# Kernel optimization log

Measured on AMD Instinct MI355X. Metric: run time of the kernel, lower is better.

## Reference

```python
import jax, jax.numpy as jnp
import numpy as np

B, T, N = 8, 168, 1024
FD, FS, FF = 16, 32, 8
DL, DG, HE, E = 128, 128, 4, 16384
BN = B * N


def _lstm_last(x, Wih, Whh, bih, bhh):
    # x: (BN, T, FD); PyTorch gate order i, f, g, o
    h0 = jnp.zeros((x.shape[0], Whh.shape[1]), x.dtype)
    def step(carry, xt):
        h, c = carry
        g = xt @ Wih.T + h @ Whh.T + bih + bhh
        i, f, gg, o = jnp.split(g, 4, axis=-1)
        c = jax.nn.sigmoid(f) * c + jax.nn.sigmoid(i) * jnp.tanh(gg)
        h = jax.nn.sigmoid(o) * jnp.tanh(c)
        return (h, c), None
    (h, _), _ = jax.lax.scan(step, (h0, h0), jnp.swapaxes(x, 0, 1))
    return h


def _ln(x, g, b):
    mu = x.mean(-1, keepdims=True)
    v = ((x - mu) ** 2).mean(-1, keepdims=True)
    return (x - mu) / jnp.sqrt(v + 1e-5) * g + b


def _gat(x, src, dst, ea, W, a_src, a_dst, a_edge, We, bias):
    # PyG GATConv: concat=False (mean over heads), edge_dim=1, LeakyReLU(0.2)
    xl = (x @ W.T).reshape(BN, HE, -1)                 # (BN, H, C)
    as_ = jnp.sum(xl * a_src, -1)                      # (BN, H)
    ad_ = jnp.sum(xl * a_dst, -1)
    ep = (ea @ We.T).reshape(-1, HE, xl.shape[-1])     # (Eb, H, C)
    ae_ = jnp.sum(ep * a_edge, -1)                     # (Eb, H)
    alpha = jax.nn.leaky_relu(as_[src] + ad_[dst] + ae_, 0.2)
    amax = jax.ops.segment_max(alpha, dst, num_segments=BN)
    ex = jnp.exp(alpha - amax[dst])
    den = jax.ops.segment_sum(ex, dst, num_segments=BN)
    w = ex / den[dst]                                  # softmax over incoming edges
    out = jax.ops.segment_sum(w[:, :, None] * xl[src], dst, num_segments=BN)
    return out.mean(axis=1) + bias


def _forward(fl, edge_index):
    (dyn, fcst, sta, ew,
     lWih, lWhh, lbih, lbhh, sW, sb, fW, fb, uW, ub,
     g0W, g0as, g0ad, g0ae, g0We, g0b,
     g1W, g1as, g1ad, g1ae, g1We, g1b,
     n0g, n0b, n1g, n1b, oW, ob) = fl
    x = jnp.transpose(dyn, (0, 2, 1, 3)).reshape(BN, T, FD)
    z = _lstm_last(x, lWih, lWhh, lbih, lbhh)
    s = jax.nn.relu(sta.reshape(BN, -1) @ sW.T + sb)
    f = jax.nn.relu(fcst.reshape(BN, -1) @ fW.T + fb)
    h = jax.nn.relu(jnp.concatenate([z, s, f], -1) @ uW.T + ub)
    # batch the graph: B disjoint copies with node offsets
    off = (jnp.arange(B) * N)[:, None]
    src = (edge_index[0][None] + off).reshape(-1)
    dst = (edge_index[1][None] + off).reshape(-1)
    ea = jnp.tile(ew.reshape(-1, 1), (B, 1))           # (B*E, 1)
    # PyG GATConv default add_self_loops=True, fill_value='mean' of incoming edge attrs
    deg = jax.ops.segment_sum(jnp.ones_like(ea), dst, num_segments=BN)
    loop_ea = jax.ops.segment_sum(ea, dst, num_segments=BN) / jnp.maximum(deg, 1.0)
    loops = jnp.arange(BN)
    src = jnp.concatenate([src, loops])
    dst = jnp.concatenate([dst, loops])
    ea = jnp.concatenate([ea, loop_ea], 0)
    # hop 0: relu on delta (not last hop), residual (res_proj=None since DL==DG), LayerNorm
    d0 = jax.nn.relu(_gat(h, src, dst, ea, g0W, g0as, g0ad, g0ae, g0We, g0b))
    h = _ln(h + d0, n0g, n0b)
    # hop 1: last hop, no relu on delta
    d1 = _gat(h, src, dst, ea, g1W, g1as, g1ad, g1ae, g1We, g1b)
    h = _ln(h + d1, n1g, n1b)
    return (h @ oW.T + ob).reshape(B, N)


def setup_inputs():
    key = jax.random.key(0)
    ks = iter(jax.random.split(key, 48))
    def rn(shape, s=0.08):
        return jax.random.normal(next(ks), shape, jnp.float32) * s
    HO = HE * DG  # heads * out_channels
    return dict(
        dynamic_features=rn((B, T, N, FD), 1.0),
        forecast_features=rn((B, N, FF), 1.0),
        static_features=rn((B, N, FS), 1.0),
        edge_index=jax.random.randint(next(ks), (2, E), 0, N),
        edge_weight=jax.random.uniform(next(ks), (E,), jnp.float32),
        lstm_Wih=rn((4 * DL, FD)), lstm_Whh=rn((4 * DL, DL)),
        lstm_bih=rn((4 * DL,)), lstm_bhh=rn((4 * DL,)),
        static_W=rn((DL, FS)), static_b=rn((DL,)),
        fcst_W=rn((DL, FF)), fcst_b=rn((DL,)),
        fusion_W=rn((DL, 3 * DL)), fusion_b=rn((DL,)),
        gat0_W=rn((HO, DL)), gat0_att_src=rn((1, HE, DG)), gat0_att_dst=rn((1, HE, DG)),
        gat0_att_edge=rn((1, HE, DG)), gat0_We=rn((HO, 1)), gat0_bias=rn((DG,)),
        gat1_W=rn((HO, DG)), gat1_att_src=rn((1, HE, DG)), gat1_att_dst=rn((1, HE, DG)),
        gat1_att_edge=rn((1, HE, DG)), gat1_We=rn((HO, 1)), gat1_bias=rn((DG,)),
        ln0_g=jnp.ones((DG,), jnp.float32), ln0_b=jnp.zeros((DG,), jnp.float32),
        ln1_g=jnp.ones((DG,), jnp.float32), ln1_b=jnp.zeros((DG,), jnp.float32),
        out_W=rn((1, DG)), out_b=rn((1,)),
    )


def reference(dynamic_features, forecast_features, static_features, edge_weight,
              lstm_Wih, lstm_Whh, lstm_bih, lstm_bhh, static_W, static_b,
              fcst_W, fcst_b, fusion_W, fusion_b,
              gat0_W, gat0_att_src, gat0_att_dst, gat0_att_edge, gat0_We, gat0_bias,
              gat1_W, gat1_att_src, gat1_att_dst, gat1_att_edge, gat1_We, gat1_bias,
              ln0_g, ln0_b, ln1_g, ln1_b, out_W, out_b, edge_index):
    fl = (dynamic_features, forecast_features, static_features, edge_weight,
          lstm_Wih, lstm_Whh, lstm_bih, lstm_bhh, static_W, static_b,
          fcst_W, fcst_b, fusion_W, fusion_b,
          gat0_W, gat0_att_src, gat0_att_dst, gat0_att_edge, gat0_We, gat0_bias,
          gat1_W, gat1_att_src, gat1_att_dst, gat1_att_edge, gat1_We, gat1_bias,
          ln0_g, ln0_b, ln1_g, ln1_b, out_W, out_b)
    return _forward(fl, edge_index)
```

## Files before the change

### kernel.cpp

```cpp
#include <hip/hip_runtime.h>
#include <hip/hip_bf16.h>
#include <stdint.h>

#define BB 8
#define TT 168
#define NN 1024
#define BN_ 8192
#define FD_ 16
#define EE 16384

typedef short short8 __attribute__((ext_vector_type(8)));
typedef __bf16 bf16x8 __attribute__((ext_vector_type(8)));
typedef float f32x4 __attribute__((ext_vector_type(4)));

#if __has_builtin(__builtin_amdgcn_exp2f)
#define EXP2(x) __builtin_amdgcn_exp2f(x)
#else
#define EXP2(x) exp2f(x)
#endif
#if __has_builtin(__builtin_amdgcn_rcpf)
#define RCPF(x) __builtin_amdgcn_rcpf(x)
#else
#define RCPF(x) (1.f / (x))
#endif
#define L2E 1.4426950408889634f
#define T2E 2.8853900817779268f

static __device__ __forceinline__ float b2f(ushort s) {
    unsigned u = ((unsigned)s) << 16;
    return __builtin_bit_cast(float, u);
}
static __device__ __forceinline__ ushort f2b(float f) {
    unsigned u = __builtin_bit_cast(unsigned, f);
    unsigned lsb = (u >> 16) & 1u;
    u += 0x7fffu + lsb;
    return (ushort)(u >> 16);
}
static __device__ __forceinline__ ushort f2b_fast(float f) {
    unsigned u = __builtin_bit_cast(unsigned, f);
    return (ushort)((u + 0x8000u) >> 16);
}
static __device__ __forceinline__ f32x4 mfma16(short8 a, short8 b, f32x4 c) {
    return __builtin_amdgcn_mfma_f32_16x16x32_bf16(
        __builtin_bit_cast(bf16x8, a), __builtin_bit_cast(bf16x8, b), c, 0, 0, 0);
}

#define O_WIH 0
#define O_WHH 8192
#define O_STA 73728
#define O_FCS 335872
#define O_SW  401408
#define O_FW  405504
#define O_UW  406528
#define O_G0W 455680
#define O_G1W 521216
#define O_END 586752

__global__ void cast_kernel(const float* __restrict__ Wih, const float* __restrict__ Whh,
                            const float* __restrict__ sta, const float* __restrict__ fcst,
                            const float* __restrict__ sW, const float* __restrict__ fW,
                            const float* __restrict__ uW, const float* __restrict__ g0W,
                            const float* __restrict__ g1W, ushort* __restrict__ dst) {
    const int i = blockIdx.x * 256 + threadIdx.x;
    if (i >= O_END) return;
    float v;
    if      (i < O_WHH) v = Wih[i - O_WIH];
    else if (i < O_STA) v = Whh[i - O_WHH];
    else if (i < O_FCS) v = sta[i - O_STA];
    else if (i < O_SW)  v = fcst[i - O_FCS];
    else if (i < O_FW)  v = sW[i - O_SW];
    else if (i < O_UW)  v = fW[i - O_FW];
    else if (i < O_G0W) v = uW[i - O_UW];
    else if (i < O_G1W) v = g0W[i - O_G0W];
    else                v = g1W[i - O_G1W];
    dst[i] = f2b(v);
}

__global__ __launch_bounds__(512, 4) void lstm_kernel(
    const float* __restrict__ dyn,
    const ushort* __restrict__ Wih,
    const ushort* __restrict__ Whh,
    const float* __restrict__ bih,
    const float* __restrict__ bhh,
    ushort* __restrict__ zsf)
{
    constexpr int HS = 168;
    __shared__ ushort hbuf[2][16 * HS];

    const int tid = threadIdx.x;
    const int blk = blockIdx.x;
    const int b = blk >> 6;
    const int n0 = (blk & 63) << 4;
    const int w = tid >> 6, lane = tid & 63, quad = lane >> 4, m = lane & 15;
    const int u = w * 16 + m;

    short8 Bf[5][4];
    float ci, cf, cg, co;
#pragma unroll
    for (int g = 0; g < 4; g++) {
        const int grow = g * 128 + u;
#pragma unroll
        for (int kt = 0; kt < 4; kt++)
            Bf[kt][g] = *(const short8*)(Whh + grow * 128 + kt * 32 + quad * 8);
        if (quad < 2) Bf[4][g] = *(const short8*)(Wih + grow * 16 + quad * 8);
        else          Bf[4][g] = short8{0, 0, 0, 0, 0, 0, 0, 0};
    }
    ci = -L2E * (bih[u] + bhh[u]);
    cf = -L2E * (bih[128 + u] + bhh[128 + u]);
    cg =  T2E * (bih[256 + u] + bhh[256 + u]);
    co = -L2E * (bih[384 + u] + bhh[384 + u]);

    float c[4];
#pragma unroll
    for (int r = 0; r < 4; r++) c[r] = 0.f;

    for (int i = tid; i < 2 * 16 * HS; i += 512) ((ushort*)hbuf)[i] = 0;
    __syncthreads();

    const int xn = tid >> 4, xf = tid & 15;
    const size_t xbase = (size_t)b * TT * NN * FD_ + (size_t)(n0 + xn) * FD_ + xf;
    float xv = 0.f;
    if (tid < 256) {
        hbuf[0][xn * HS + 128 + xf] = f2b(dyn[xbase]);
        xv = dyn[xbase + (size_t)NN * FD_];
    }
    __syncthreads();

    for (int t = 0; t < TT; t++) {
        const ushort* rb = hbuf[t & 1];
        ushort* wb = hbuf[(t + 1) & 1];
        if (tid < 256) {
            if (t + 1 < TT) wb[xn * HS + 128 + xf] = f2b(xv);
            if (t + 2 < TT) xv = dyn[xbase + (size_t)(t + 2) * NN * FD_];
        }

        f32x4 acc[4];
#pragma unroll
        for (int g = 0; g < 4; g++) acc[g] = f32x4{0.f, 0.f, 0.f, 0.f};
#pragma unroll
        for (int kt = 0; kt < 5; kt++) {
            short8 a = *(const short8*)&rb[m * HS + kt * 32 + quad * 8];
#pragma unroll
            for (int g = 0; g < 4; g++)
                acc[g] = mfma16(a, Bf[kt][g], acc[g]);
        }

#pragma unroll
        for (int r = 0; r < 4; r++) {
            const int n = quad * 4 + r;
            const float Di = 1.f + EXP2(fmaf(acc[0][r], -L2E, ci));
            const float Df = 1.f + EXP2(fmaf(acc[1][r], -L2E, cf));
            const float Eg = EXP2(fmaf(acc[2][r], T2E, cg));
            const float Do = 1.f + EXP2(fmaf(acc[3][r], -L2E, co));
            const float R  = RCPF(Di * (1.f + Eg));
            const float sf = RCPF(Df);
            const float cc = fmaf(sf, c[r], (Eg - 1.f) * R);
            c[r] = cc;
            const float Ec = EXP2(T2E * cc);
            const float h = (Ec - 1.f) * RCPF(Do * (1.f + Ec));
            wb[n * HS + u] = f2b_fast(h);
            if (t == TT - 1) zsf[(size_t)(blk * 16 + n) * 384 + u] = f2b_fast(h);
        }
        __syncthreads();
    }
}

__global__ __launch_bounds__(256) void gemm_sf_prep_kernel(
    const ushort* __restrict__ staB, const ushort* __restrict__ sWB,
    const float* __restrict__ sb,
    const ushort* __restrict__ fcsB, const ushort* __restrict__ fWB,
    const float* __restrict__ fb, ushort* __restrict__ zsf,
    const int* __restrict__ ei, const float* __restrict__ ew,
    const float* __restrict__ We0, const float* __restrict__ ae0,
    const float* __restrict__ We1, const float* __restrict__ ae1,
    int* __restrict__ deg0, int* __restrict__ offs, float* __restrict__ loopea,
    int* __restrict__ eidx, float* __restrict__ se) {
    const int tid = threadIdx.x;
    if (blockIdx.x < 2048) {
        const int lane = tid & 63, quad = lane >> 4, m = lane & 15;
        int wave = blockIdx.x * 4 + (tid >> 6);
        const short8 z8 = short8{0, 0, 0, 0, 0, 0, 0, 0};
        short8 a, bf;
        int r0, c0, ocol;
        const float* bias;
        if (wave < 4096) {
            r0 = (wave >> 3) * 16; c0 = (wave & 7) * 16; ocol = 128; bias = sb;
            a  = *(const short8*)(staB + (size_t)(r0 + m) * 32 + quad * 8);
            bf = *(const short8*)(sWB + (size_t)(c0 + m) * 32 + quad * 8);
        } else {
            wave -= 4096;
            r0 = (wave >> 3) * 16; c0 = (wave & 7) * 16; ocol = 256; bias = fb;
            a  = (quad == 0) ? *(const short8*)(fcsB + (size_t)(r0 + m) * 8) : z8;
            bf = (quad == 0) ? *(const short8*)(fWB + (size_t)(c0 + m) * 8) : z8;
        }
        f32x4 acc = mfma16(a, bf, f32x4{0.f, 0.f, 0.f, 0.f});
        const float bv = bias[c0 + m];
#pragma unroll
        for (int r = 0; r < 4; r++) {
            const int row = r0 + quad * 4 + r;
            zsf[(size_t)row * 384 + ocol + c0 + m] = f2b(fmaxf(acc[r] + bv, 0.f));
        }
        return;
    }
    __shared__ int degL[1024];
    __shared__ float wsL[1024];
    __shared__ int part[256];
    __shared__ float seL[8];
    for (int i = tid; i < 1024; i += 256) { degL[i] = 0; wsL[i] = 0.f; }
    if (tid < 8) seL[tid] = 0.f;
    __syncthreads();
    for (int e = tid; e < EE; e += 256) {
        const int d = ei[EE + e];
        atomicAdd(&degL[d], 1);
        atomicAdd(&wsL[d], ew[e]);
    }
    __syncthreads();
    const int d0 = degL[4 * tid], d1 = degL[4 * tid + 1];
    const int d2 = degL[4 * tid + 2], d3 = degL[4 * tid + 3];
    const int tot = d0 + d1 + d2 + d3;
    part[tid] = tot;
    __syncthreads();
    for (int o = 1; o < 256; o <<= 1) {
        const int v = (tid >= o) ? part[tid - o] : 0;
        __syncthreads();
        part[tid] += v;
        __syncthreads();
    }
    int base = part[tid] - tot;
    int ex[4];
    ex[0] = base; ex[1] = base + d0; ex[2] = ex[1] + d1; ex[3] = ex[2] + d2;
    const int dd4[4] = {d0, d1, d2, d3};
#pragma unroll
    for (int j = 0; j < 4; j++) {
        const int n = 4 * tid + j;
        offs[n] = ex[j];
        deg0[n] = dd4[j];
        loopea[n] = wsL[n] / fmaxf((float)dd4[j], 1.f);
    }
    __syncthreads();
#pragma unroll
    for (int j = 0; j < 4; j++) degL[4 * tid + j] = ex[j];
    __syncthreads();
    for (int e = tid; e < EE; e += 256) {
        const int dd = ei[EE + e];
        const int slot = atomicAdd(&degL[dd], 1);
        eidx[slot] = e;
    }
    for (int i = tid; i < 1024; i += 256) {
        const int g = i >> 7, k = i & 127, head = g & 3;
        const float* W = (g >> 2) ? We1 : We0;
        const float* A = (g >> 2) ? ae1 : ae0;
        atomicAdd(&seL[g], W[head * 128 + k] * A[head * 128 + k]);
    }
    __syncthreads();
    if (tid < 8) se[tid] = seL[tid];
}

__global__ __launch_bounds__(256) void gemm_fusion_kernel(
    const ushort* __restrict__ A, const ushort* __restrict__ Bt,
    const float* __restrict__ bias, ushort* __restrict__ hB, float* __restrict__ hF) {
    const int tid = threadIdx.x;
    const int lane = tid & 63, quad = lane >> 4, m = lane & 15;
    const int wave = blockIdx.x * 4 + (tid >> 6);
    const int r0 = (wave >> 3) * 16, c0 = (wave & 7) * 16;
    f32x4 acc = f32x4{0.f, 0.f, 0.f, 0.f};
#pragma unroll
    for (int kt = 0; kt < 12; kt++) {
        const int k = kt * 32 + quad * 8;
        short8 a  = *(const short8*)(A + (size_t)(r0 + m) * 384 + k);
        short8 bf = *(const short8*)(Bt + (size_t)(c0 + m) * 384 + k);
        acc = mfma16(a, bf, acc);
    }
    const int col = c0 + m;
    const float bv = bias[col];
#pragma unroll
    for (int r = 0; r < 4; r++) {
        const int row = r0 + quad * 4 + r;
        const float v = fmaxf(acc[r] + bv, 0.f);
        hB[(size_t)row * 128 + col] = f2b(v);
        hF[(size_t)row * 128 + col] = v;
    }
}

__global__ __launch_bounds__(256) void gemmatt_kernel(
    const ushort* __restrict__ hB, const ushort* __restrict__ W,
    const float* __restrict__ asrc, const float* __restrict__ adst,
    ushort* __restrict__ xl, float* __restrict__ as_, float* __restrict__ ad_) {
    const int tid = threadIdx.x;
    const int lane = tid & 63, quad = lane >> 4, m = lane & 15;
    const int w = tid >> 6;
    const int r0 = blockIdx.x * 16;
    f32x4 acc[8];
#pragma unroll
    for (int ct = 0; ct < 8; ct++) acc[ct] = f32x4{0.f, 0.f, 0.f, 0.f};
#pragma unroll
    for (int kt = 0; kt < 4; kt++) {
        const int k = kt * 32 + quad * 8;
        short8 a = *(const short8*)(hB + (size_t)(r0 + m) * 128 + k);
#pragma unroll
        for (int ct = 0; ct < 8; ct++) {
            short8 bf = *(const short8*)(W + (size_t)(w * 128 + ct * 16 + m) * 128 + k);
            acc[ct] = mfma16(a, bf, acc[ct]);
        }
    }
    float sa[4] = {0.f, 0.f, 0.f, 0.f}, sd[4] = {0.f, 0.f, 0.f, 0.f};
#pragma unroll
    for (int ct = 0; ct < 8; ct++) {
        const int col = w * 128 + ct * 16 + m;
        const float av = asrc[col], dv = adst[col];
#pragma unroll
        for (int r = 0; r < 4; r++) {
            const float v = acc[ct][r];
            xl[(size_t)(r0 + quad * 4 + r) * 512 + col] = f2b(v);
            sa[r] = fmaf(v, av, sa[r]);
            sd[r] = fmaf(v, dv, sd[r]);
        }
    }
#pragma unroll
    for (int o = 1; o < 16; o <<= 1) {
#pragma unroll
        for (int r = 0; r < 4; r++) {
            sa[r] += __shfl_xor(sa[r], o);
            sd[r] += __shfl_xor(sd[r], o);
        }
    }
    if (m == 0) {
#pragma unroll
        for (int r = 0; r < 4; r++) {
            const int node = r0 + quad * 4 + r;
            as_[node * 4 + w] = sa[r];
            ad_[node * 4 + w] = sd[r];
        }
    }
}

__global__ __launch_bounds__(256) void gat_kernel(
    float* __restrict__ hF, ushort* __restrict__ hB, const ushort* __restrict__ xl,
    const float* __restrict__ as_, const float* __restrict__ ad_,
    const int* __restrict__ eidx, const int* __restrict__ offs,
    const int* __restrict__ deg0, const float* __restrict__ loopea,
    const int* __restrict__ ei, const float* __restrict__ ew,
    const float* __restrict__ se4, const float* __restrict__ bias,
    const float* __restrict__ lng, const float* __restrict__ lnb, int relu,
    int writeOut, const float* __restrict__ oW, const float* __restrict__ ob,
    float* __restrict__ out) {
    const int lane = threadIdx.x & 63;
    const int v = blockIdx.x * 4 + (threadIdx.x >> 6);
    const int b = v >> 10, n = v & 1023;
    const int dg = deg0[n], off = offs[n];

    float se[4];
#pragma unroll
    for (int h = 0; h < 4; h++) se[h] = se4[h];

    const float lea = loopea[n];
    const float4 s4 = *(const float4*)(as_ + v * 4);
    const float4 d4 = *(const float4*)(ad_ + v * 4);
    const float* sp = (const float*)&s4;
    const float* dp = (const float*)&d4;
    float den[4], num0[4], num1[4];
#pragma unroll
    for (int h = 0; h < 4; h++) {
        float a = sp[h] + dp[h] + lea * se[h];
        a = (a < 0.f) ? 0.2f * a : a;
        const float p = EXP2(fminf(a, 60.f) * L2E);
        den[h] = p;
        num0[h] = p * b2f(xl[(size_t)v * 512 + h * 128 + lane]);
        num1[h] = p * b2f(xl[(size_t)v * 512 + h * 128 + 64 + lane]);
    }
    for (int i = 0; i < dg; i++) {
        const int e = eidx[off + i];
        const int src = b * 1024 + ei[e];
        const float eaw = ew[e];
        const float4 ss4 = *(const float4*)(as_ + src * 4);
        const float* ssp = (const float*)&ss4;
        const ushort* xr = xl + (size_t)src * 512;
#pragma unroll
        for (int h = 0; h < 4; h++) {
            float a = ssp[h] + dp[h] + eaw * se[h];
            a = (a < 0.f) ? 0.2f * a : a;
            const float p = EXP2(fminf(a, 60.f) * L2E);
            den[h] += p;
            num0[h] = fmaf(p, b2f(xr[h * 128 + lane]), num0[h]);
            num1[h] = fmaf(p, b2f(xr[h * 128 + 64 + lane]), num1[h]);
        }
    }
    float o0 = 0.f, o1 = 0.f;
#pragma unroll
    for (int h = 0; h < 4; h++) {
        const float inv = RCPF(den[h]);
        o0 = fmaf(num0[h], inv, o0);
        o1 = fmaf(num1[h], inv, o1);
    }

    float d0 = o0 * 0.25f + bias[lane];
    float d1 = o1 * 0.25f + bias[64 + lane];
    if (relu) { d0 = fmaxf(d0, 0.f); d1 = fmaxf(d1, 0.f); }
    const float x0 = hF[(size_t)v * 128 + lane] + d0;
    const float x1 = hF[(size_t)v * 128 + 64 + lane] + d1;

    float s = x0 + x1;
#pragma unroll
    for (int o = 32; o; o >>= 1) s += __shfl_xor(s, o);
    const float mu = s * (1.f / 128.f);
    const float e0 = x0 - mu, e1 = x1 - mu;
    float vs = e0 * e0 + e1 * e1;
#pragma unroll
    for (int o = 32; o; o >>= 1) vs += __shfl_xor(vs, o);
    const float r = rsqrtf(vs * (1.f / 128.f) + 1e-5f);
    const float y0 = e0 * r * lng[lane] + lnb[lane];
    const float y1 = e1 * r * lng[64 + lane] + lnb[64 + lane];
    if (writeOut) {
        float t = y0 * oW[lane] + y1 * oW[64 + lane];
#pragma unroll
        for (int o = 32; o; o >>= 1) t += __shfl_xor(t, o);
        if (lane == 0) out[v] = t + ob[0];
    } else {
        hF[(size_t)v * 128 + lane] = y0;
        hF[(size_t)v * 128 + 64 + lane] = y1;
        hB[(size_t)v * 128 + lane] = f2b(y0);
        hB[(size_t)v * 128 + 64 + lane] = f2b(y1);
    }
}

extern "C" void kernel_launch(void* const* d_in, const int* in_sizes, int n_in,
                              void* d_out, int out_size, void* d_ws, size_t ws_size,
                              hipStream_t stream) {
    const float* dyn  = (const float*)d_in[0];
    const float* fcst = (const float*)d_in[1];
    const float* sta  = (const float*)d_in[2];
    const int*   ei   = (const int*)d_in[3];
    const float* ew   = (const float*)d_in[4];
    const float* lWih = (const float*)d_in[5];
    const float* lWhh = (const float*)d_in[6];
    const float* lbih = (const float*)d_in[7];
    const float* lbhh = (const float*)d_in[8];
    const float* sW = (const float*)d_in[9];
    const float* sb = (const float*)d_in[10];
    const float* fW = (const float*)d_in[11];
    const float* fb = (const float*)d_in[12];
    const float* uW = (const float*)d_in[13];
    const float* ub = (const float*)d_in[14];
    const float* g0W  = (const float*)d_in[15];
    const float* g0as = (const float*)d_in[16];
    const float* g0ad = (const float*)d_in[17];
    const float* g0ae = (const float*)d_in[18];
    const float* g0We = (const float*)d_in[19];
    const float* g0b  = (const float*)d_in[20];
    const float* g1W  = (const float*)d_in[21];
    const float* g1as = (const float*)d_in[22];
    const float* g1ad = (const float*)d_in[23];
    const float* g1ae = (const float*)d_in[24];
    const float* g1We = (const float*)d_in[25];
    const float* g1b  = (const float*)d_in[26];
    const float* ln0g = (const float*)d_in[27];
    const float* ln0b = (const float*)d_in[28];
    const float* ln1g = (const float*)d_in[29];
    const float* ln1b = (const float*)d_in[30];
    const float* oW = (const float*)d_in[31];
    const float* ob = (const float*)d_in[32];

    char* p = (char*)d_ws;
    ushort* castB = (ushort*)p; p += (size_t)O_END * 2 + 512;
    ushort* zsf = (ushort*)p;  p += (size_t)BN_ * 384 * 2;
    float*  hF  = (float*)p;   p += (size_t)BN_ * 128 * 4;
    ushort* hB  = (ushort*)p;  p += (size_t)BN_ * 128 * 2;
    ushort* xl  = (ushort*)p;  p += (size_t)BN_ * 512 * 2;
    float*  asb = (float*)p;   p += (size_t)BN_ * 4 * 4;
    float*  adb = (float*)p;   p += (size_t)BN_ * 4 * 4;
    int*    deg0   = (int*)p;   p += 4096;
    int*    offs   = (int*)p;   p += 4096;
    float*  loopea = (float*)p; p += 4096;
    int*    eidx   = (int*)p;   p += (size_t)EE * 4;
    float*  se     = (float*)p; p += 256;

    const ushort* WihB = castB + O_WIH;
    const ushort* WhhB = castB + O_WHH;
    const ushort* staB = castB + O_STA;
    const ushort* fcsB = castB + O_FCS;
    const ushort* sWB  = castB + O_SW;
    const ushort* fWB  = castB + O_FW;
    const ushort* uWB  = castB + O_UW;
    const ushort* g0WB = castB + O_G0W;
    const ushort* g1WB = castB + O_G1W;

    cast_kernel<<<(O_END + 255) / 256, 256, 0, stream>>>(lWih, lWhh, sta, fcst, sW, fW,
                                                         uW, g0W, g1W, castB);
    lstm_kernel<<<512, 512, 0, stream>>>(dyn, WihB, WhhB, lbih, lbhh, zsf);
    gemm_sf_prep_kernel<<<2049, 256, 0, stream>>>(staB, sWB, sb, fcsB, fWB, fb, zsf,
                                                  ei, ew, g0We, g0ae, g1We, g1ae,
                                                  deg0, offs, loopea, eidx, se);
    gemm_fusion_kernel<<<1024, 256, 0, stream>>>(zsf, uWB, ub, hB, hF);

    gemmatt_kernel<<<512, 256, 0, stream>>>(hB, g0WB, g0as, g0ad, xl, asb, adb);
    gat_kernel<<<2048, 256, 0, stream>>>(hF, hB, xl, asb, adb, eidx, offs, deg0,
                                         loopea, ei, ew, se, g0b, ln0g, ln0b, 1,
                                         0, oW, ob, (float*)d_out);
    gemmatt_kernel<<<512, 256, 0, stream>>>(hB, g1WB, g1as, g1ad, xl, asb, adb);
    gat_kernel<<<2048, 256, 0, stream>>>(hF, hB, xl, asb, adb, eidx, offs, deg0,
                                         loopea, ei, ew, se + 4, g1b, ln1g, ln1b, 0,
                                         1, oW, ob, (float*)d_out);
}
```

Measured before the change: 605.1 us.

## Halve LSTM block threads with two unit tiles per wave and interleave xl heads

```diff
diff --git a/kernel.cpp b/kernel.cpp
--- a/kernel.cpp
+++ b/kernel.cpp
@@ -76,7 +76,7 @@
     dst[i] = f2b(v);
 }
 
-__global__ __launch_bounds__(512, 4) void lstm_kernel(
+__global__ __launch_bounds__(256, 2) void lstm_kernel(
     const float* __restrict__ dyn,
     const ushort* __restrict__ Wih,
     const ushort* __restrict__ Whh,
@@ -92,74 +92,100 @@
     const int b = blk >> 6;
     const int n0 = (blk & 63) << 4;
     const int w = tid >> 6, lane = tid & 63, quad = lane >> 4, m = lane & 15;
-    const int u = w * 16 + m;
-
-    short8 Bf[5][4];
-    float ci, cf, cg, co;
-#pragma unroll
-    for (int g = 0; g < 4; g++) {
-        const int grow = g * 128 + u;
-#pragma unroll
-        for (int kt = 0; kt < 4; kt++)
-            Bf[kt][g] = *(const short8*)(Whh + grow * 128 + kt * 32 + quad * 8);
-        if (quad < 2) Bf[4][g] = *(const short8*)(Wih + grow * 16 + quad * 8);
-        else          Bf[4][g] = short8{0, 0, 0, 0, 0, 0, 0, 0};
-    }
-    ci = -L2E * (bih[u] + bhh[u]);
-    cf = -L2E * (bih[128 + u] + bhh[128 + u]);
-    cg =  T2E * (bih[256 + u] + bhh[256 + u]);
-    co = -L2E * (bih[384 + u] + bhh[384 + u]);
-
-    float c[4];
-#pragma unroll
-    for (int r = 0; r < 4; r++) c[r] = 0.f;
-
-    for (int i = tid; i < 2 * 16 * HS; i += 512) ((ushort*)hbuf)[i] = 0;
+
+    short8 Bf[5][4][2];
+    float ci[2][4], cf[2][4], cg[2][4], co[2][4];
+#pragma unroll
+    for (int jj = 0; jj < 2; jj++) {
+        const int ua = (2 * w + jj) * 16 + m;
+#pragma unroll
+        for (int g = 0; g < 4; g++) {
+            const int grow = g * 128 + ua;
+#pragma unroll
+            for (int kt = 0; kt < 4; kt++)
+                Bf[kt][g][jj] = *(const short8*)(Whh + grow * 128 + kt * 32 + quad * 8);
+            if (quad < 2) Bf[4][g][jj] = *(const short8*)(Wih + grow * 16 + quad * 8);
+            else          Bf[4][g][jj] = short8{0, 0, 0, 0, 0, 0, 0, 0};
+        }
+        const int u0 = (2 * w + jj) * 16 + quad * 4;
+        const float4 bi4 = *(const float4*)(bih + u0);
+        const float4 bh4 = *(const float4*)(bhh + u0);
+        const float4 fi4 = *(const float4*)(bih + 128 + u0);
+        const float4 fh4 = *(const float4*)(bhh + 128 + u0);
+        const float4 gi4 = *(const float4*)(bih + 256 + u0);
+        const float4 gh4 = *(const float4*)(bhh + 256 + u0);
+        const float4 oi4 = *(const float4*)(bih + 384 + u0);
+        const float4 oh4 = *(const float4*)(bhh + 384 + u0);
+        const float* bi = (const float*)&bi4; const float* bh = (const float*)&bh4;
+        const float* fi = (const float*)&fi4; const float* fh = (const float*)&fh4;
+        const float* gi = (const float*)&gi4; const float* gh = (const float*)&gh4;
+        const float* oi = (const float*)&oi4; const float* oh = (const float*)&oh4;
+#pragma unroll
+        for (int r = 0; r < 4; r++) {
+            ci[jj][r] = -L2E * (bi[r] + bh[r]);
+            cf[jj][r] = -L2E * (fi[r] + fh[r]);
+            cg[jj][r] =  T2E * (gi[r] + gh[r]);
+            co[jj][r] = -L2E * (oi[r] + oh[r]);
+        }
+    }
+
+    float c[2][4];
+#pragma unroll
+    for (int jj = 0; jj < 2; jj++)
+#pragma unroll
+        for (int r = 0; r < 4; r++) c[jj][r] = 0.f;
+
+    for (int i = tid; i < 2 * 16 * HS; i += 256) ((ushort*)hbuf)[i] = 0;
     __syncthreads();
 
     const int xn = tid >> 4, xf = tid & 15;
     const size_t xbase = (size_t)b * TT * NN * FD_ + (size_t)(n0 + xn) * FD_ + xf;
-    float xv = 0.f;
-    if (tid < 256) {
-        hbuf[0][xn * HS + 128 + xf] = f2b(dyn[xbase]);
-        xv = dyn[xbase + (size_t)NN * FD_];
-    }
+    hbuf[0][xn * HS + 128 + xf] = f2b(dyn[xbase]);
+    float xv = dyn[xbase + (size_t)NN * FD_];
     __syncthreads();
 
     for (int t = 0; t < TT; t++) {
         const ushort* rb = hbuf[t & 1];
         ushort* wb = hbuf[(t + 1) & 1];
-        if (tid < 256) {
-            if (t + 1 < TT) wb[xn * HS + 128 + xf] = f2b(xv);
-            if (t + 2 < TT) xv = dyn[xbase + (size_t)(t + 2) * NN * FD_];
-        }
-
-        f32x4 acc[4];
-#pragma unroll
-        for (int g = 0; g < 4; g++) acc[g] = f32x4{0.f, 0.f, 0.f, 0.f};
+        if (t + 1 < TT) wb[xn * HS + 128 + xf] = f2b(xv);
+        if (t + 2 < TT) xv = dyn[xbase + (size_t)(t + 2) * NN * FD_];
+
+        f32x4 acc[4][2];
+#pragma unroll
+        for (int g = 0; g < 4; g++)
+#pragma unroll
+            for (int jj = 0; jj < 2; jj++) acc[g][jj] = f32x4{0.f, 0.f, 0.f, 0.f};
 #pragma unroll
         for (int kt = 0; kt < 5; kt++) {
             short8 a = *(const short8*)&rb[m * HS + kt * 32 + quad * 8];
 #pragma unroll
             for (int g = 0; g < 4; g++)
-                acc[g] = mfma16(a, Bf[kt][g], acc[g]);
-        }
-
-#pragma unroll
-        for (int r = 0; r < 4; r++) {
-            const int n = quad * 4 + r;
-            const float Di = 1.f + EXP2(fmaf(acc[0][r], -L2E, ci));
-            const float Df = 1.f + EXP2(fmaf(acc[1][r], -L2E, cf));
-            const float Eg = EXP2(fmaf(acc[2][r], T2E, cg));
-            const float Do = 1.f + EXP2(fmaf(acc[3][r], -L2E, co));
-            const float R  = RCPF(Di * (1.f + Eg));
-            const float sf = RCPF(Df);
-            const float cc = fmaf(sf, c[r], (Eg - 1.f) * R);
-            c[r] = cc;
-            const float Ec = EXP2(T2E * cc);
-            const float h = (Ec - 1.f) * RCPF(Do * (1.f + Ec));
-            wb[n * HS + u] = f2b_fast(h);
-            if (t == TT - 1) zsf[(size_t)(blk * 16 + n) * 384 + u] = f2b_fast(h);
+#pragma unroll
+                for (int jj = 0; jj < 2; jj++)
+                    acc[g][jj] = mfma16(Bf[kt][g][jj], a, acc[g][jj]);
+        }
+
+#pragma unroll
+        for (int jj = 0; jj < 2; jj++) {
+            const int u0 = (2 * w + jj) * 16 + quad * 4;
+            ushort4 hv;
+#pragma unroll
+            for (int r = 0; r < 4; r++) {
+                const float Di = 1.f + EXP2(fmaf(acc[0][jj][r], -L2E, ci[jj][r]));
+                const float Df = 1.f + EXP2(fmaf(acc[1][jj][r], -L2E, cf[jj][r]));
+                const float Eg = EXP2(fmaf(acc[2][jj][r], T2E, cg[jj][r]));
+                const float Do = 1.f + EXP2(fmaf(acc[3][jj][r], -L2E, co[jj][r]));
+                const float R  = RCPF(Di * (1.f + Eg));
+                const float sf = RCPF(Df);
+                const float cc = fmaf(sf, c[jj][r], (Eg - 1.f) * R);
+                c[jj][r] = cc;
+                const float Ec = EXP2(T2E * cc);
+                const float h = (Ec - 1.f) * RCPF(Do * (1.f + Ec));
+                hv[r] = f2b_fast(h);
+            }
+            *(ushort4*)&wb[m * HS + u0] = hv;
+            if (t == TT - 1)
+                *(ushort4*)&zsf[(size_t)(blk * 16 + m) * 384 + u0] = hv;
         }
         __syncthreads();
     }
@@ -306,12 +332,12 @@
     float sa[4] = {0.f, 0.f, 0.f, 0.f}, sd[4] = {0.f, 0.f, 0.f, 0.f};
 #pragma unroll
     for (int ct = 0; ct < 8; ct++) {
-        const int col = w * 128 + ct * 16 + m;
-        const float av = asrc[col], dv = adst[col];
+        const int c = ct * 16 + m;
+        const float av = asrc[w * 128 + c], dv = adst[w * 128 + c];
 #pragma unroll
         for (int r = 0; r < 4; r++) {
             const float v = acc[ct][r];
-            xl[(size_t)(r0 + quad * 4 + r) * 512 + col] = f2b(v);
+            xl[(size_t)(r0 + quad * 4 + r) * 512 + c * 4 + w] = f2b(v);
             sa[r] = fmaf(v, av, sa[r]);
             sd[r] = fmaf(v, dv, sd[r]);
         }
@@ -359,14 +385,20 @@
     const float* sp = (const float*)&s4;
     const float* dp = (const float*)&d4;
     float den[4], num0[4], num1[4];
-#pragma unroll
-    for (int h = 0; h < 4; h++) {
-        float a = sp[h] + dp[h] + lea * se[h];
-        a = (a < 0.f) ? 0.2f * a : a;
-        const float p = EXP2(fminf(a, 60.f) * L2E);
-        den[h] = p;
-        num0[h] = p * b2f(xl[(size_t)v * 512 + h * 128 + lane]);
-        num1[h] = p * b2f(xl[(size_t)v * 512 + h * 128 + 64 + lane]);
+    {
+        const ushort4 xa = *(const ushort4*)(xl + (size_t)v * 512 + lane * 4);
+        const ushort4 xb = *(const ushort4*)(xl + (size_t)v * 512 + (64 + lane) * 4);
+        const ushort* xap = (const ushort*)&xa;
+        const ushort* xbp = (const ushort*)&xb;
+#pragma unroll
+        for (int h = 0; h < 4; h++) {
+            float a = sp[h] + dp[h] + lea * se[h];
+            a = (a < 0.f) ? 0.2f * a : a;
+            const float p = EXP2(fminf(a, 60.f) * L2E);
+            den[h] = p;
+            num0[h] = p * b2f(xap[h]);
+            num1[h] = p * b2f(xbp[h]);
+        }
     }
     for (int i = 0; i < dg; i++) {
         const int e = eidx[off + i];
@@ -374,15 +406,18 @@
         const float eaw = ew[e];
         const float4 ss4 = *(const float4*)(as_ + src * 4);
         const float* ssp = (const float*)&ss4;
-        const ushort* xr = xl + (size_t)src * 512;
+        const ushort4 xa = *(const ushort4*)(xl + (size_t)src * 512 + lane * 4);
+        const ushort4 xb = *(const ushort4*)(xl + (size_t)src * 512 + (64 + lane) * 4);
+        const ushort* xap = (const ushort*)&xa;
+        const ushort* xbp = (const ushort*)&xb;
 #pragma unroll
         for (int h = 0; h < 4; h++) {
             float a = ssp[h] + dp[h] + eaw * se[h];
             a = (a < 0.f) ? 0.2f * a : a;
             const float p = EXP2(fminf(a, 60.f) * L2E);
             den[h] += p;
-            num0[h] = fmaf(p, b2f(xr[h * 128 + lane]), num0[h]);
-            num1[h] = fmaf(p, b2f(xr[h * 128 + 64 + lane]), num1[h]);
+            num0[h] = fmaf(p, b2f(xap[h]), num0[h]);
+            num1[h] = fmaf(p, b2f(xbp[h]), num1[h]);
         }
     }
     float o0 = 0.f, o1 = 0.f;
@@ -486,7 +521,7 @@
 
     cast_kernel<<<(O_END + 255) / 256, 256, 0, stream>>>(lWih, lWhh, sta, fcst, sW, fW,
                                                          uW, g0W, g1W, castB);
-    lstm_kernel<<<512, 512, 0, stream>>>(dyn, WihB, WhhB, lbih, lbhh, zsf);
+    lstm_kernel<<<512, 256, 0, stream>>>(dyn, WihB, WhhB, lbih, lbhh, zsf);
     gemm_sf_prep_kernel<<<2049, 256, 0, stream>>>(staB, sWB, sb, fcsB, fWB, fb, zsf,
                                                   ei, ew, g0We, g0ae, g1We, g1ae,
                                                   deg0, offs, loopea, eidx, se);
```

New measurement: 650.2 us. 7.4% more time.
